# Kernel tuning notes

Measured on AMD Instinct MI355X. Metric: run time of the kernel, lower is better.

Reference implementation:

```python
import jax, jax.numpy as jnp
import numpy as np

D_MODEL = 512
N_HEADS = 8
D_FF = 1024
LV = 2048
LT = 512
GAMMA = 0.9
SCALE_BASE = 512  # XPOS default scale_base


def _dup_interleave(m):
    # (L, d/2) -> (L, d) duplicating each column: [a,b] -> [a,a,b,b]
    return jnp.repeat(m, 2, axis=-1)


def _xpos(x, downscale=False):
    # XPOS rotary embedding (RetNet-style), x: (B, L, d)
    B, L, d = x.shape
    half = d // 2
    s = (jnp.arange(0, d, 2, dtype=jnp.float32) + 0.4 * d) / (1.4 * d)  # (d/2,)
    scale = s[None, :] ** (jnp.arange(L, dtype=jnp.float32)[:, None] / SCALE_BASE)  # (L, d/2)
    inv_freq = 1.0 / (10000.0 ** (jnp.arange(half, dtype=jnp.float32) / half))
    ang = jnp.arange(L, dtype=jnp.float32)[:, None] * inv_freq[None, :]  # (L, d/2)
    if downscale:
        scale = 1.0 / scale
    sin = _dup_interleave(jnp.sin(ang) * scale)[None]  # (1, L, d)
    cos = _dup_interleave(jnp.cos(ang) * scale)[None]
    x1, x2 = x[..., 0::2], x[..., 1::2]
    rot = jnp.stack((-x2, x1), axis=-1).reshape(x.shape)  # rotate_every_two
    return x * cos + rot * sin


def _sine_pos(L, d):
    # DETR-style normalized 1D sine position embedding, mask = ones(1, L)
    x_embed = jnp.arange(1, L + 1, dtype=jnp.float32)  # cumsum of ones
    x_embed = x_embed / (x_embed[-1] + 1e-6) * (2.0 * np.pi)
    dim_t = jnp.arange(d, dtype=jnp.float32)
    dim_t = 10000.0 ** (2.0 * jnp.floor(dim_t / 2.0) / d)
    pos = x_embed[:, None] / dim_t[None, :]  # (L, d)
    pos = jnp.stack((jnp.sin(pos[:, 0::2]), jnp.cos(pos[:, 1::2])), axis=2).reshape(L, d)
    return pos[None]  # (1, L, d)


def _ln(x, w, b, eps=1e-5):
    mu = jnp.mean(x, axis=-1, keepdims=True)
    var = jnp.var(x, axis=-1, keepdims=True)
    return (x - mu) / jnp.sqrt(var + eps) * w + b


def _ret_forward(src_vid, src_txt, ln1_w, ln1_b, wq, bq, wk, bk, wv, bv, wo, bo,
                 lin1_w, lin1_b, lin2_w, lin2_b, ln2_w, ln2_b, ln3_w, ln3_b,
                 learn_ret_w):
    B, Lv, D = src_vid.shape
    Lt = src_txt.shape[1]
    h, dk = N_HEADS, D // N_HEADS

    # retention decay matrix D[n,m] = gamma^(n-m) for n>=m else 0
    n = jnp.arange(Lv)
    delta = jnp.maximum(n[:, None] - n[None, :], 0).astype(jnp.float32)
    Dm = jnp.where(n[:, None] >= n[None, :], GAMMA ** delta, 0.0)

    # learned sparse mask
    learn = jax.nn.sigmoid(learn_ret_w.reshape(Lv, Lv))
    diag = jnp.eye(Lv, dtype=jnp.float32)
    video_ret = (1.0 - diag) * learn
    learn_mask = diag + video_ret
    mask = Dm * learn_mask  # mask_choice == 'both'
    loss_sparsity = jnp.mean(jnp.abs(video_ret))

    # position encodings
    pos_vid_q = _xpos(src_vid)
    pos_vid_k = _xpos(src_vid, downscale=True)
    pos_txt = _sine_pos(Lt, D)
    src = jnp.concatenate([src_vid, src_txt], axis=1)       # (B, Lv+Lt, D)
    pos = jnp.concatenate([pos_vid_q, pos_txt], axis=1)
    pos_k = jnp.concatenate([pos_vid_k, pos_txt], axis=1)

    # --- RetLayer (eval mode: dropout = identity) ---
    src2 = _ln(src, ln1_w, ln1_b)
    q = src2[:, :Lv] + pos[:, :Lv]
    k = src2[:, :Lv] + pos_k[:, :Lv]
    v = src2[:, :Lv]

    # multi-head attention with MULTIPLICATIVE mask on logits
    qh = (q @ wq.T + bq).reshape(B, Lv, h, dk) / jnp.sqrt(jnp.float32(dk))
    kh = (k @ wk.T + bk).reshape(B, Lv, h, dk)
    vh = (v @ wv.T + bv).reshape(B, Lv, h, dk)
    attn = jnp.einsum('blhd,bmhd->bhlm', qh, kh) * mask[None, None]
    attn = jax.nn.softmax(attn, axis=-1)
    vid_att = jnp.einsum('bhlm,bmhd->blhd', attn, vh).reshape(B, Lv, D)
    vid_att = vid_att @ wo.T + bo

    src2 = jnp.concatenate([vid_att, src2[:, Lv:]], axis=1) + pos
    src = src + src2
    src2 = _ln(src, ln2_w, ln2_b)
    src2 = jax.nn.gelu(src2 @ lin1_w.T + lin1_b, approximate=False) @ lin2_w.T + lin2_b
    src = src + src2
    src = _ln(src, ln3_w, ln3_b)
    return src[:, :Lv], src[:, Lv:], loss_sparsity


def setup_inputs() -> dict:
    key = jax.random.key(0)
    ks = jax.random.split(key, 12)
    D, F = D_MODEL, D_FF
    w = lambda k, shp: (jax.random.normal(k, shp, dtype=jnp.float32) * 0.02)
    return {
        'src_vid': jax.random.normal(ks[0], (1, LV, D), dtype=jnp.float32),
        'src_txt': jax.random.normal(ks[1], (1, LT, D), dtype=jnp.float32),
        'ln1_w': jnp.ones((D,), jnp.float32), 'ln1_b': jnp.zeros((D,), jnp.float32),
        'wq': w(ks[2], (D, D)), 'bq': jnp.zeros((D,), jnp.float32),
        'wk': w(ks[3], (D, D)), 'bk': jnp.zeros((D,), jnp.float32),
        'wv': w(ks[4], (D, D)), 'bv': jnp.zeros((D,), jnp.float32),
        'wo': w(ks[5], (D, D)), 'bo': jnp.zeros((D,), jnp.float32),
        'lin1_w': w(ks[6], (F, D)), 'lin1_b': jnp.zeros((F,), jnp.float32),
        'lin2_w': w(ks[7], (D, F)), 'lin2_b': jnp.zeros((D,), jnp.float32),
        'ln2_w': jnp.ones((D,), jnp.float32), 'ln2_b': jnp.zeros((D,), jnp.float32),
        'ln3_w': jnp.ones((D,), jnp.float32), 'ln3_b': jnp.zeros((D,), jnp.float32),
        'learn_ret_w': jax.random.normal(ks[8], (LV * LV,), dtype=jnp.float32),
    }


def reference(src_vid, src_txt, ln1_w, ln1_b, wq, bq, wk, bk, wv, bv, wo, bo,
              lin1_w, lin1_b, lin2_w, lin2_b, ln2_w, ln2_b, ln3_w, ln3_b,
              learn_ret_w):
    return _ret_forward(src_vid, src_txt, ln1_w, ln1_b, wq, bq, wk, bk, wv, bv,
                        wo, bo, lin1_w, lin1_b, lin2_w, lin2_b, ln2_w, ln2_b,
                        ln3_w, ln3_b, learn_ret_w)
```

## Files before the change

kernel.cpp:

```cpp
#include <hip/hip_runtime.h>
#include <hip/hip_bf16.h>
#include <math.h>

#define LVID 2048
#define LTXT 512
#define DMOD 512
#define LTOT 2560
#define LOG2_GAMMA (-0.15200309344504995f)
#define LOG2E 1.4426950408889634f

typedef __bf16 bf16x8 __attribute__((ext_vector_type(8)));
typedef float f32x4 __attribute__((ext_vector_type(4)));

__device__ inline f32x4 mfma_bf16(bf16x8 a, bf16x8 b, f32x4 c) {
  return __builtin_amdgcn_mfma_f32_16x16x32_bf16(a, b, c, 0, 0, 0);
}

__device__ inline void gload_lds16(const void* g, void* l) {
  __builtin_amdgcn_global_load_lds(
      (const __attribute__((address_space(1))) void*)g,
      (__attribute__((address_space(3))) void*)l, 16, 0, 0);
}

union U8 { __hip_bfloat16 b[8]; uint4 u; };

__global__ __launch_bounds__(256) void k_prep_ln1(
    const float* __restrict__ lw, float* __restrict__ premask2,
    float* __restrict__ lossp,
    const float* __restrict__ wq, const float* __restrict__ wk,
    const float* __restrict__ wv, const float* __restrict__ wo,
    const float* __restrict__ l1, const float* __restrict__ l2,
    __hip_bfloat16* __restrict__ dst,
    const float* __restrict__ src_vid, const float* __restrict__ src_txt,
    const float* __restrict__ w, const float* __restrict__ b,
    __hip_bfloat16* __restrict__ acat, float* __restrict__ srcA,
    float* __restrict__ posb) {
  int tid = threadIdx.x;
  int blk = blockIdx.x;
  if (blk < 2048) {
    __shared__ float red[256];
    int i = blk;
    int i0r = i & ~63;
    int tloCol = (i0r > 900) ? (((i0r - 900) >> 6) << 6) : 0;
    int idx0 = (blk * 256 + tid) * 8;
    int j0 = idx0 & 2047;
    float4 lv0 = *(const float4*)&lw[idx0];
    float4 lv1 = *(const float4*)&lw[idx0 + 4];
    float lvv[8] = {lv0.x, lv0.y, lv0.z, lv0.w, lv1.x, lv1.y, lv1.z, lv1.w};
    float pm[8];
    float s = 0.f;
#pragma unroll
    for (int e = 0; e < 8; e++) {
      int j = j0 + e;
      float sig = 1.f / (1.f + __expf(-lvv[e]));
      if (j != i) s += sig;
      float m = (j > i) ? 0.f
              : ((j == i) ? 1.f : exp2f((float)(i - j) * LOG2_GAMMA) * sig);
      pm[e] = m * LOG2E;
    }
    if (j0 >= tloCol && j0 < i0r + 64) {
      *(float4*)&premask2[idx0]     = *(float4*)&pm[0];
      *(float4*)&premask2[idx0 + 4] = *(float4*)&pm[4];
    }
    red[tid] = s; __syncthreads();
    for (int st = 128; st > 0; st >>= 1) { if (tid < st) red[tid] += red[tid + st]; __syncthreads(); }
    if (tid == 0) lossp[blk] = red[0];
  } else if (blk < 4096) {
    int i4 = (blk - 2048) * 256 + tid;
    const float* sp; int base;
    if (i4 < 131072)      { if (i4 < 65536)  { sp = wq; base = 0; }      else { sp = wk; base = 65536; } }
    else if (i4 < 262144) { if (i4 < 196608) { sp = wv; base = 131072; } else { sp = wo; base = 196608; } }
    else if (i4 < 393216) { sp = l1; base = 262144; }
    else                  { sp = l2; base = 393216; }
    float4 v = ((const float4*)sp)[i4 - base];
    __hip_bfloat16 o[4] = {__float2bfloat16(v.x), __float2bfloat16(v.y),
                           __float2bfloat16(v.z), __float2bfloat16(v.w)};
    *(uint2*)(dst + (size_t)i4 * 4) = *(uint2*)o;
  } else {
    int row = (blk - 4096) * 4 + (tid >> 6);
    int lane = tid & 63;
    const float* xs = (row < LVID) ? (src_vid + (size_t)row * DMOD)
                                   : (src_txt + (size_t)(row - LVID) * DMOD);
    float x[8];
    { float4 v0 = *(const float4*)&xs[lane * 8];
      float4 v1 = *(const float4*)&xs[lane * 8 + 4];
      x[0]=v0.x; x[1]=v0.y; x[2]=v0.z; x[3]=v0.w;
      x[4]=v1.x; x[5]=v1.y; x[6]=v1.z; x[7]=v1.w; }
    float s = 0.f;
#pragma unroll
    for (int i = 0; i < 8; i++) s += x[i];
#pragma unroll
    for (int st = 1; st < 64; st <<= 1) s += __shfl_xor(s, st, 64);
    float mu = s * (1.f / DMOD);
    float vs = 0.f;
#pragma unroll
    for (int i = 0; i < 8; i++) { float d = x[i] - mu; vs += d * d; }
#pragma unroll
    for (int st = 1; st < 64; st <<= 1) vs += __shfl_xor(vs, st, 64);
    float inv = rsqrtf(vs * (1.f / DMOD) + 1e-5f);
    float y[8];
    { float4 w0 = *(const float4*)&w[lane * 8];
      float4 w1 = *(const float4*)&w[lane * 8 + 4];
      float4 b0 = *(const float4*)&b[lane * 8];
      float4 b1 = *(const float4*)&b[lane * 8 + 4];
      float wv_[8] = {w0.x,w0.y,w0.z,w0.w,w1.x,w1.y,w1.z,w1.w};
      float bv_[8] = {b0.x,b0.y,b0.z,b0.w,b1.x,b1.y,b1.z,b1.w};
#pragma unroll
      for (int i = 0; i < 8; i++) y[i] = (x[i] - mu) * inv * wv_[i] + bv_[i]; }
    size_t base = (size_t)row * DMOD + lane * 8;
    if (row < LVID) {
      U8 pv;
#pragma unroll
      for (int i = 0; i < 8; i++) pv.b[i] = __float2bfloat16(y[i]);
      *(uint4*)&acat[(size_t)(4096 + row) * DMOD + lane * 8] = pv.u;
      float pq[8], pk[8];
      float l = (float)row;
#pragma unroll
      for (int p = 0; p < 4; p++) {
        int j = lane * 4 + p;
        float sj = (2.f * j + 204.8f) * (1.f / 716.8f);
        float scale = __powf(sj, l * (1.f / 512.f));
        float invfreq = __powf(10000.f, -(float)j * (1.f / 256.f));
        float sn, cs; __sincosf(l * invfreq, &sn, &cs);
        float cq = cs * scale, sq = sn * scale;
        pq[2*p]   = x[2*p] * cq - x[2*p+1] * sq;
        pq[2*p+1] = x[2*p+1] * cq + x[2*p] * sq;
        float isc = 1.f / scale;
        float ck = cs * isc, sk = sn * isc;
        pk[2*p]   = x[2*p] * ck - x[2*p+1] * sk;
        pk[2*p+1] = x[2*p+1] * ck + x[2*p] * sk;
      }
      *(float4*)&posb[base]     = *(float4*)&pq[0];
      *(float4*)&posb[base + 4] = *(float4*)&pq[4];
      U8 pqv, pkv;
#pragma unroll
      for (int i = 0; i < 8; i++) {
        pqv.b[i] = __float2bfloat16(y[i] + pq[i]);
        pkv.b[i] = __float2bfloat16(y[i] + pk[i]);
      }
      *(uint4*)&acat[(size_t)row * DMOD + lane * 8] = pqv.u;
      *(uint4*)&acat[(size_t)(2048 + row) * DMOD + lane * 8] = pkv.u;
    } else {
      int l = row - LVID;
      float xe = (float)(l + 1) * (6.28318530717958647692f / 512.000001f);
      float o8[8];
#pragma unroll
      for (int p = 0; p < 4; p++) {
        int j = lane * 4 + p;
        float dimt = __powf(10000.f, (float)j * (1.f / 256.f));
        float a = xe / dimt;
        o8[2*p]   = x[2*p]   + y[2*p]   + __sinf(a);
        o8[2*p+1] = x[2*p+1] + y[2*p+1] + __cosf(a);
      }
      *(float4*)&srcA[base]     = *(float4*)&o8[0];
      *(float4*)&srcA[base + 4] = *(float4*)&o8[4];
    }
  }
}

__global__ __launch_bounds__(256) void k_ln2(
    const float* __restrict__ srcA,
    const float* __restrict__ w, const float* __restrict__ b,
    __hip_bfloat16* __restrict__ obf) {
  int row = blockIdx.x * 4 + (threadIdx.x >> 6);
  int lane = threadIdx.x & 63;
  size_t base = (size_t)row * DMOD + lane * 8;
  float x[8];
  { float4 v0 = *(const float4*)&srcA[base];
    float4 v1 = *(const float4*)&srcA[base + 4];
    x[0]=v0.x; x[1]=v0.y; x[2]=v0.z; x[3]=v0.w;
    x[4]=v1.x; x[5]=v1.y; x[6]=v1.z; x[7]=v1.w; }
  float s = 0.f;
#pragma unroll
  for (int i = 0; i < 8; i++) s += x[i];
#pragma unroll
  for (int st = 1; st < 64; st <<= 1) s += __shfl_xor(s, st, 64);
  float mu = s * (1.f / DMOD);
  float vs = 0.f;
#pragma unroll
  for (int i = 0; i < 8; i++) { float d = x[i] - mu; vs += d * d; }
#pragma unroll
  for (int st = 1; st < 64; st <<= 1) vs += __shfl_xor(vs, st, 64);
  float inv = rsqrtf(vs * (1.f / DMOD) + 1e-5f);
  float4 w0 = *(const float4*)&w[lane * 8];
  float4 w1 = *(const float4*)&w[lane * 8 + 4];
  float4 b0 = *(const float4*)&b[lane * 8];
  float4 b1 = *(const float4*)&b[lane * 8 + 4];
  float wv_[8] = {w0.x,w0.y,w0.z,w0.w,w1.x,w1.y,w1.z,w1.w};
  float bv_[8] = {b0.x,b0.y,b0.z,b0.w,b1.x,b1.y,b1.z,b1.w};
  U8 o;
#pragma unroll
  for (int i = 0; i < 8; i++)
    o.b[i] = __float2bfloat16((x[i] - mu) * inv * wv_[i] + bv_[i]);
  *(uint4*)&obf[base] = o.u;
}

__global__ __launch_bounds__(256) void k_ln3(
    const float* __restrict__ srcA, const float* __restrict__ ffo0,
    const float* __restrict__ ffo1,
    const float* __restrict__ w, const float* __restrict__ b,
    float* __restrict__ o, const float* __restrict__ lossp) {
  if (blockIdx.x == 0 && threadIdx.x < 64) {
    float s = 0.f;
    for (int i = threadIdx.x; i < 2048; i += 64) s += lossp[i];
#pragma unroll
    for (int st = 1; st < 64; st <<= 1) s += __shfl_xor(s, st, 64);
    if (threadIdx.x == 0) o[1310720] = s * (1.f / 4194304.f);
  }
  int row = blockIdx.x * 4 + (threadIdx.x >> 6);
  int lane = threadIdx.x & 63;
  size_t base = (size_t)row * DMOD + lane * 8;
  float x[8];
  { float4 a0 = *(const float4*)&srcA[base];
    float4 a1 = *(const float4*)&srcA[base + 4];
    float4 f0 = *(const float4*)&ffo0[base];
    float4 f1 = *(const float4*)&ffo0[base + 4];
    float4 g0 = *(const float4*)&ffo1[base];
    float4 g1 = *(const float4*)&ffo1[base + 4];
    x[0]=a0.x+f0.x+g0.x; x[1]=a0.y+f0.y+g0.y; x[2]=a0.z+f0.z+g0.z; x[3]=a0.w+f0.w+g0.w;
    x[4]=a1.x+f1.x+g1.x; x[5]=a1.y+f1.y+g1.y; x[6]=a1.z+f1.z+g1.z; x[7]=a1.w+f1.w+g1.w; }
  float s = 0.f;
#pragma unroll
  for (int i = 0; i < 8; i++) s += x[i];
#pragma unroll
  for (int st = 1; st < 64; st <<= 1) s += __shfl_xor(s, st, 64);
  float mu = s * (1.f / DMOD);
  float vs = 0.f;
#pragma unroll
  for (int i = 0; i < 8; i++) { float d = x[i] - mu; vs += d * d; }
#pragma unroll
  for (int st = 1; st < 64; st <<= 1) vs += __shfl_xor(vs, st, 64);
  float inv = rsqrtf(vs * (1.f / DMOD) + 1e-5f);
  float4 w0 = *(const float4*)&w[lane * 8];
  float4 w1 = *(const float4*)&w[lane * 8 + 4];
  float4 b0 = *(const float4*)&b[lane * 8];
  float4 b1 = *(const float4*)&b[lane * 8 + 4];
  float wv_[8] = {w0.x,w0.y,w0.z,w0.w,w1.x,w1.y,w1.z,w1.w};
  float bv_[8] = {b0.x,b0.y,b0.z,b0.w,b1.x,b1.y,b1.z,b1.w};
  float y[8];
#pragma unroll
  for (int i = 0; i < 8; i++) y[i] = (x[i] - mu) * inv * wv_[i] + bv_[i];
  *(float4*)&o[base]     = *(float4*)&y[0];
  *(float4*)&o[base + 4] = *(float4*)&y[4];
}

template <int EPI>
__global__ __launch_bounds__(256) void k_gemm4(
    const __hip_bfloat16* __restrict__ A, const __hip_bfloat16* __restrict__ W0,
    const float* __restrict__ b0, const float* __restrict__ b1,
    const float* __restrict__ b2, void* __restrict__ Cv,
    const float* __restrict__ res1, const float* __restrict__ res2,
    __hip_bfloat16* __restrict__ vT, float* __restrict__ vts,
    int M, int N, int K) {
  __shared__ __hip_bfloat16 sA[2][2048];
  __shared__ __hip_bfloat16 sB[2][2048];
  int tid = threadIdx.x, lane = tid & 63, w = tid >> 6;
  int c16 = lane & 15, q4 = lane >> 4;
  int bm = blockIdx.y * 64, bn = blockIdx.x * 64;
  int seg = (EPI == 3) ? (bm >> 11) : 0;
  const __hip_bfloat16* Wp = (EPI == 3) ? (W0 + (size_t)seg * ((size_t)N * K)) : W0;
  int kb   = (EPI == 5) ? (int)blockIdx.z * (K >> 1) : 0;
  int Keff = (EPI == 5) ? (K >> 1) : K;
  int r0 = tid >> 2, cc0 = (tid & 3) * 8;
  const __hip_bfloat16* gA = A  + (size_t)(bm + r0) * K + kb + cc0;
  const __hip_bfloat16* gB = Wp + (size_t)(bn + r0) * K + kb + cc0;
  auto stage = [&](int buf, int k0) {
    gload_lds16(gA + k0, &sA[buf][(size_t)tid * 8]);
    gload_lds16(gB + k0, &sB[buf][(size_t)tid * 8]);
  };
  f32x4 acc[2][2];
  { f32x4 z = {0.f,0.f,0.f,0.f}; acc[0][0]=z; acc[0][1]=z; acc[1][0]=z; acc[1][1]=z; }
  int wm = w & 1, wn = w >> 1;
  const int S = Keff >> 5;
  stage(0, 0);
  for (int s = 0; s < S; s++) {
    __syncthreads();
    if (s + 1 < S) stage((s + 1) & 1, (s + 1) * 32);
    int bf = s & 1;
    bf16x8 af[2], bfr[2];
    af[0]  = *(const bf16x8*)&sA[bf][(wm*32 + c16) * 32 + q4*8];
    af[1]  = *(const bf16x8*)&sA[bf][(wm*32 + 16 + c16) * 32 + q4*8];
    bfr[0] = *(const bf16x8*)&sB[bf][(wn*32 + c16) * 32 + q4*8];
    bfr[1] = *(const bf16x8*)&sB[bf][(wn*32 + 16 + c16) * 32 + q4*8];
    acc[0][0] = mfma_bf16(af[0], bfr[0], acc[0][0]);
    acc[0][1] = mfma_bf16(af[0], bfr[1], acc[0][1]);
    acc[1][0] = mfma_bf16(af[1], bfr[0], acc[1][0]);
    acc[1][1] = mfma_bf16(af[1], bfr[1], acc[1][1]);
  }
  float alpha = (EPI == 3 && seg == 0) ? 0.125f : 1.f;
  const float* bp = (EPI == 3) ? (seg == 0 ? b0 : (seg == 1 ? b1 : b2)) : b0;
  if (EPI == 3 && seg == 2) {
    int tile = (bm & 2047) >> 6;
    float vsum[2] = {0.f, 0.f};
#pragma unroll
    for (int j = 0; j < 2; j++) {
      int n = bn + wn*32 + j*16 + c16;
      float bs = bp[n];
#pragma unroll
      for (int i = 0; i < 2; i++) {
        ushort4 u; float vv[4];
#pragma unroll
        for (int r = 0; r < 4; r++) {
          __hip_bfloat16 vb = __float2bfloat16(acc[i][j][r] + bs);
          ((__hip_bfloat16*)&u)[r] = vb;
          vv[r] = __bfloat162float(vb);
        }
        int jj = (bm & 2047) + wm*32 + i*16 + q4*4;
        *(ushort4*)&vT[(size_t)n * 2048 + jj] = u;
        vsum[j] += vv[0] + vv[1] + vv[2] + vv[3];
      }
    }
#pragma unroll
    for (int j = 0; j < 2; j++) {
      float s2 = vsum[j];
      s2 += __shfl_xor(s2, 16, 64);
      s2 += __shfl_xor(s2, 32, 64);
      int n = bn + wn*32 + j*16 + c16;
      if (q4 == 0) atomicAdd(&vts[(size_t)(n >> 6) * 2048 + tile * 64 + (n & 63)], s2);
    }
    return;
  }
  float vdummy;
  (void)vdummy;
#pragma unroll
  for (int j = 0; j < 2; j++) {
    int n = bn + wn*32 + j*16 + c16;
    float bs = bp[n];
    if (EPI == 5 && blockIdx.z != 0) bs = 0.f;
#pragma unroll
    for (int i = 0; i < 2; i++) {
#pragma unroll
      for (int r = 0; r < 4; r++) {
        int m = bm + wm*32 + i*16 + q4*4 + r;
        float v = (acc[i][j][r] + bs) * alpha;
        if (EPI == 4) v = 0.5f * v * (1.f + erff(v * 0.70710678118654752f));
        if (EPI == 2) {
          size_t off = (size_t)m * N + n;
          ((float*)Cv)[off] = v + res1[off] + res2[off];
        } else if (EPI == 4) {
          ((__hip_bfloat16*)Cv)[(size_t)m * N + n] = __float2bfloat16(v);
        } else if (EPI == 5) {
          ((float*)Cv)[(size_t)blockIdx.z * 1310720 + (size_t)m * N + n] = v;
        } else {
          ((__hip_bfloat16*)Cv)[(size_t)(m & 2047) * 1024 + seg * 512 + n] = __float2bfloat16(v);
        }
      }
    }
  }
}

__global__ __launch_bounds__(256) void k_attn(
    const __hip_bfloat16* __restrict__ qkb,
    const float* __restrict__ premask2,
    const __hip_bfloat16* __restrict__ vT,
    __hip_bfloat16* __restrict__ Obuf,
    float* __restrict__ ml) {
  __shared__ __hip_bfloat16 sQ[64][72];
  __shared__ __hip_bfloat16 sK[2][64][72];
  __shared__ __hip_bfloat16 sVt[2][64][72];
  __shared__ __hip_bfloat16 sP[64][72];
  int i0 = blockIdx.x * 64, h = blockIdx.y, z = blockIdx.z;
  int tid = threadIdx.x, lane = tid & 63, w = tid >> 6;
  int c16 = lane & 15, q4 = lane >> 4;
  {
    int r = tid >> 2, c0 = (tid & 3) * 16;
    const __hip_bfloat16* g = qkb + (size_t)(i0 + r) * 1024 + h * 64 + c0;
    *(uint4*)&sQ[r][c0]     = *(const uint4*)g;
    *(uint4*)&sQ[r][c0 + 8] = *(const uint4*)(g + 8);
  }
  int thi = i0 >> 6;
  int tlo = (i0 > 900) ? ((i0 - 900) >> 6) : 0;
  int n = thi - tlo + 1;
  int t0 = z ? (tlo + (n >> 1)) : tlo;
  int t1 = z ? thi : (tlo + (n >> 1) - 1);
  float rm = 0.f, rz = 0.f;
  f32x4 O[4];
  { f32x4 zz = {0.f,0.f,0.f,0.f}; O[0]=zz; O[1]=zz; O[2]=zz; O[3]=zz; }
  int kr = tid >> 2, kc = (tid & 3) * 16;
  uint4 pk0, pk1, pv0, pv1;
  if (t0 <= t1) {
    const __hip_bfloat16* gk = qkb + (size_t)(t0*64 + kr) * 1024 + 512 + h*64 + kc;
    pk0 = *(const uint4*)gk; pk1 = *(const uint4*)(gk + 8);
    const __hip_bfloat16* gv = vT + (size_t)(h*64 + kr) * 2048 + t0*64 + kc;
    pv0 = *(const uint4*)gv; pv1 = *(const uint4*)(gv + 8);
  }
  for (int t = t0; t <= t1; t++) {
    int buf = (t - t0) & 1;
    *(uint4*)&sK[buf][kr][kc]      = pk0;
    *(uint4*)&sK[buf][kr][kc + 8]  = pk1;
    *(uint4*)&sVt[buf][kr][kc]     = pv0;
    *(uint4*)&sVt[buf][kr][kc + 8] = pv1;
    __syncthreads();
    if (t < t1) {
      const __hip_bfloat16* gk = qkb + (size_t)((t+1)*64 + kr) * 1024 + 512 + h*64 + kc;
      pk0 = *(const uint4*)gk; pk1 = *(const uint4*)(gk + 8);
      const __hip_bfloat16* gv = vT + (size_t)(h*64 + kr) * 2048 + (t+1)*64 + kc;
      pv0 = *(const uint4*)gv; pv1 = *(const uint4*)(gv + 8);
    }
    bf16x8 bq0 = *(const bf16x8*)&sQ[w*16 + c16][q4*8];
    bf16x8 bq1 = *(const bf16x8*)&sQ[w*16 + c16][32 + q4*8];
    f32x4 St[4];
#pragma unroll
    for (int jt = 0; jt < 4; jt++) {
      f32x4 zz = {0.f,0.f,0.f,0.f};
      bf16x8 a0 = *(const bf16x8*)&sK[buf][jt*16 + c16][q4*8];
      bf16x8 a1 = *(const bf16x8*)&sK[buf][jt*16 + c16][32 + q4*8];
      zz = mfma_bf16(a0, bq0, zz);
      zz = mfma_bf16(a1, bq1, zz);
      St[jt] = zz;
    }
    int qg = i0 + w*16 + c16;
    float lg[4][4];
    float tmax = -3.0e38f;
#pragma unroll
    for (int jt = 0; jt < 4; jt++) {
      float4 pm = *(const float4*)&premask2[(size_t)qg * 2048 + t*64 + jt*16 + q4*4];
      lg[jt][0] = St[jt][0] * pm.x; lg[jt][1] = St[jt][1] * pm.y;
      lg[jt][2] = St[jt][2] * pm.z; lg[jt][3] = St[jt][3] * pm.w;
#pragma unroll
      for (int r = 0; r < 4; r++) tmax = fmaxf(tmax, lg[jt][r]);
    }
    tmax = fmaxf(tmax, __shfl_xor(tmax, 16, 64));
    tmax = fmaxf(tmax, __shfl_xor(tmax, 32, 64));
    float mn = fmaxf(rm, tmax);
    float al = exp2f(rm - mn);
    rm = mn;
    float zp = 0.f;
#pragma unroll
    for (int jt = 0; jt < 4; jt++) {
      U8 e4;
      float e0 = exp2f(lg[jt][0] - rm), e1 = exp2f(lg[jt][1] - rm);
      float e2 = exp2f(lg[jt][2] - rm), e3 = exp2f(lg[jt][3] - rm);
      zp += e0 + e1 + e2 + e3;
      e4.b[0] = __float2bfloat16(e0); e4.b[1] = __float2bfloat16(e1);
      e4.b[2] = __float2bfloat16(e2); e4.b[3] = __float2bfloat16(e3);
      *(uint2*)&sP[w*16 + c16][jt*16 + q4*4] = *(uint2*)&e4.b[0];
    }
    zp += __shfl_xor(zp, 16, 64);
    zp += __shfl_xor(zp, 32, 64);
    rz = rz * al + zp;
    float alr[4];
#pragma unroll
    for (int r = 0; r < 4; r++) alr[r] = __shfl(al, q4*4 + r, 64);
#pragma unroll
    for (int dt = 0; dt < 4; dt++)
#pragma unroll
      for (int r = 0; r < 4; r++) O[dt][r] *= alr[r];
    bf16x8 ap0 = *(const bf16x8*)&sP[w*16 + c16][q4*8];
    bf16x8 ap1 = *(const bf16x8*)&sP[w*16 + c16][32 + q4*8];
#pragma unroll
    for (int dt = 0; dt < 4; dt++) {
      bf16x8 bv0 = *(const bf16x8*)&sVt[buf][dt*16 + c16][q4*8];
      bf16x8 bv1 = *(const bf16x8*)&sVt[buf][dt*16 + c16][32 + q4*8];
      O[dt] = mfma_bf16(ap0, bv0, O[dt]);
      O[dt] = mfma_bf16(ap1, bv1, O[dt]);
    }
  }
  __hip_bfloat16* ob = Obuf + (size_t)z * (2048 * 512);
#pragma unroll
  for (int dt = 0; dt < 4; dt++) {
    int d = dt*16 + c16;
#pragma unroll
    for (int r = 0; r < 4; r++)
      ob[(size_t)(i0 + w*16 + q4*4 + r) * DMOD + h*64 + d] = __float2bfloat16(O[dt][r]);
  }
  if (q4 == 0) {
    size_t mi = (((size_t)z * 8 + h) * 2048 + i0 + w*16 + c16) * 2;
    ml[mi] = rm; ml[mi + 1] = rz;
  }
}

__global__ __launch_bounds__(256) void k_comb(
    const __hip_bfloat16* __restrict__ Obuf, const float* __restrict__ ml,
    const float* __restrict__ vts,
    __hip_bfloat16* __restrict__ outp) {
  __shared__ float sV[32][64];
  __shared__ float sS[64];
  __shared__ float sC[64][4];
  int i0 = blockIdx.x * 64, h = blockIdx.y;
  int tid = threadIdx.x;
  int thi = i0 >> 6;
  int tlo = (i0 > 900) ? ((i0 - 900) >> 6) : 0;
  int n = thi - tlo + 1;
  float nu = (float)(2048 - 64 * n);
  {
    const float4* src = (const float4*)(vts + (size_t)h * 2048);
    ((float4*)&sV[0][0])[tid * 2]     = src[tid * 2];
    ((float4*)&sV[0][0])[tid * 2 + 1] = src[tid * 2 + 1];
  }
  __syncthreads();
  if (tid < 64) {
    float s = 0.f;
    for (int t = 0; t < 32; t++) if (t < tlo || t > thi) s += sV[t][tid];
    sS[tid] = s;
  } else if (tid < 128) {
    int r = tid - 64;
    int row = i0 + r;
    float m0 = ml[(((size_t)0 * 8 + h) * 2048 + row) * 2];
    float l0 = ml[(((size_t)0 * 8 + h) * 2048 + row) * 2 + 1];
    float m1 = ml[(((size_t)1 * 8 + h) * 2048 + row) * 2];
    float l1 = ml[(((size_t)1 * 8 + h) * 2048 + row) * 2 + 1];
    float M = fmaxf(m0, m1);
    float a0 = exp2f(m0 - M), a1 = exp2f(m1 - M), au = exp2f(-M);
    float dinv = 1.f / (l0 * a0 + l1 * a1 + nu * au);
    sC[r][0] = a0 * dinv; sC[r][1] = a1 * dinv; sC[r][2] = au * dinv;
  }
  __syncthreads();
  int r = tid >> 2, dc = (tid & 3) * 16;
  size_t off = (size_t)(i0 + r) * DMOD + h * 64 + dc;
  U8 o0a, o0b, o1a, o1b, oa, obb;
  o0a.u = *(const uint4*)&Obuf[off];
  o0b.u = *(const uint4*)&Obuf[off + 8];
  o1a.u = *(const uint4*)&Obuf[(size_t)2048 * 512 + off];
  o1b.u = *(const uint4*)&Obuf[(size_t)2048 * 512 + off + 8];
  float c0 = sC[r][0], c1 = sC[r][1], cu = sC[r][2];
#pragma unroll
  for (int k = 0; k < 8; k++) {
    float v = __bfloat162float(o0a.b[k]) * c0 + __bfloat162float(o1a.b[k]) * c1
            + sS[dc + k] * cu;
    oa.b[k] = __float2bfloat16(v);
  }
#pragma unroll
  for (int k = 0; k < 8; k++) {
    float v = __bfloat162float(o0b.b[k]) * c0 + __bfloat162float(o1b.b[k]) * c1
            + sS[dc + 8 + k] * cu;
    obb.b[k] = __float2bfloat16(v);
  }
  *(uint4*)&outp[off]     = oa.u;
  *(uint4*)&outp[off + 8] = obb.u;
}

extern "C" void kernel_launch(void* const* d_in, const int* in_sizes, int n_in,
                              void* d_out, int out_size, void* d_ws, size_t ws_size,
                              hipStream_t stream) {
  const float* src_vid = (const float*)d_in[0];
  const float* src_txt = (const float*)d_in[1];
  const float* ln1_w = (const float*)d_in[2];
  const float* ln1_b = (const float*)d_in[3];
  const float* wq = (const float*)d_in[4];
  const float* bq = (const float*)d_in[5];
  const float* wk = (const float*)d_in[6];
  const float* bk = (const float*)d_in[7];
  const float* wv = (const float*)d_in[8];
  const float* bv = (const float*)d_in[9];
  const float* wo = (const float*)d_in[10];
  const float* bo = (const float*)d_in[11];
  const float* lin1_w = (const float*)d_in[12];
  const float* lin1_b = (const float*)d_in[13];
  const float* lin2_w = (const float*)d_in[14];
  const float* lin2_b = (const float*)d_in[15];
  const float* ln2_w = (const float*)d_in[16];
  const float* ln2_b = (const float*)d_in[17];
  const float* ln3_w = (const float*)d_in[18];
  const float* ln3_b = (const float*)d_in[19];
  const float* lw = (const float*)d_in[20];
  float* out = (float*)d_out;

  const size_t MB = 1048576;
  char* wsb = (char*)d_ws;
  float* premask2       = (float*)(wsb + 0);
  __hip_bfloat16* wqb   = (__hip_bfloat16*)(wsb + 16*MB);
  __hip_bfloat16* wob   = wqb + 786432;
  __hip_bfloat16* l1b   = wqb + 1048576;
  __hip_bfloat16* l2b   = wqb + 1572864;
  __hip_bfloat16* acat  = (__hip_bfloat16*)(wsb + 20*MB);
  __hip_bfloat16* qkb   = (__hip_bfloat16*)(wsb + 26*MB);
  __hip_bfloat16* vTb   = (__hip_bfloat16*)(wsb + 30*MB);
  __hip_bfloat16* Obuf  = (__hip_bfloat16*)(wsb + 32*MB);
  float* mlb            = (float*)(wsb + 36*MB);
  float* vts            = (float*)(wsb + 37*MB);
  __hip_bfloat16* vattb = (__hip_bfloat16*)(wsb + 38*MB);
  float* srcA           = (float*)(wsb + 40*MB);
  float* posb           = (float*)(wsb + 45*MB);
  __hip_bfloat16* s2b   = (__hip_bfloat16*)(wsb + 50*MB);
  __hip_bfloat16* hidb  = (__hip_bfloat16*)(wsb + 53*MB);
  float* ffo0           = (float*)(wsb + 58*MB);
  float* ffo1           = (float*)(wsb + 63*MB);
  float* lossp          = (float*)(wsb + 68*MB);

  hipMemsetAsync(vts, 0, 8 * 32 * 64 * sizeof(float), stream);

  k_prep_ln1<<<4736, 256, 0, stream>>>(lw, premask2, lossp,
      wq, wk, wv, wo, lin1_w, lin2_w, wqb,
      src_vid, src_txt, ln1_w, ln1_b, acat, srcA, posb);

  k_gemm4<3><<<dim3(8, 96), 256, 0, stream>>>(acat, wqb, bq, bk, bv,
      qkb, nullptr, nullptr, vTb, vts, 6144, 512, 512);
  k_attn<<<dim3(32, 8, 2), 256, 0, stream>>>(qkb, premask2, vTb, Obuf, mlb);
  k_comb<<<dim3(32, 8), 256, 0, stream>>>(Obuf, mlb, vts, vattb);
  k_gemm4<2><<<dim3(8, 32), 256, 0, stream>>>(vattb, wob, bo, nullptr, nullptr,
      srcA, src_vid, posb, nullptr, nullptr, 2048, 512, 512);
  k_ln2<<<640, 256, 0, stream>>>(srcA, ln2_w, ln2_b, s2b);
  k_gemm4<4><<<dim3(16, 40), 256, 0, stream>>>(s2b, l1b, lin1_b, nullptr, nullptr,
      hidb, nullptr, nullptr, nullptr, nullptr, 2560, 1024, 512);
  k_gemm4<5><<<dim3(8, 40, 2), 256, 0, stream>>>(hidb, l2b, lin2_b, nullptr, nullptr,
      ffo0, nullptr, nullptr, nullptr, nullptr, 2560, 512, 1024);
  k_ln3<<<640, 256, 0, stream>>>(srcA, ffo0, ffo1, ln3_w, ln3_b, out, lossp);
}
```

Measured before the change: 216.1 us.

## Split attention KV range four ways, deepen GEMM k-step, fold vts memset

Attention blocks now split each query tile's key-tile range into four partitions instead of two. The combine kernel merges four partial softmax states plus the uniform term, and the workspace layout is enlarged to hold four Obuf slices. The GEMM kernel stages 64-wide K chunks per barrier instead of 32, halving synchronisation count at the cost of doubled LDS. The separate memset of vts is folded into the first prep kernel to drop one launch. This risks more partial-result traffic in the combine step.

```diff
diff --git a/kernel.cpp b/kernel.cpp
--- a/kernel.cpp
+++ b/kernel.cpp
@@ -26,7 +26,7 @@
 
 __global__ __launch_bounds__(256) void k_prep_ln1(
     const float* __restrict__ lw, float* __restrict__ premask2,
-    float* __restrict__ lossp,
+    float* __restrict__ lossp, float* __restrict__ vts,
     const float* __restrict__ wq, const float* __restrict__ wk,
     const float* __restrict__ wv, const float* __restrict__ wo,
     const float* __restrict__ l1, const float* __restrict__ l2,
@@ -37,6 +37,7 @@
     float* __restrict__ posb) {
   int tid = threadIdx.x;
   int blk = blockIdx.x;
+  if (blk < 64) vts[blk * 256 + tid] = 0.f;
   if (blk < 2048) {
     __shared__ float red[256];
     int i = blk;
@@ -245,15 +246,15 @@
 }
 
 template <int EPI>
-__global__ __launch_bounds__(256) void k_gemm4(
+__global__ __launch_bounds__(256) void k_gemm5(
     const __hip_bfloat16* __restrict__ A, const __hip_bfloat16* __restrict__ W0,
     const float* __restrict__ b0, const float* __restrict__ b1,
     const float* __restrict__ b2, void* __restrict__ Cv,
     const float* __restrict__ res1, const float* __restrict__ res2,
     __hip_bfloat16* __restrict__ vT, float* __restrict__ vts,
     int M, int N, int K) {
-  __shared__ __hip_bfloat16 sA[2][2048];
-  __shared__ __hip_bfloat16 sB[2][2048];
+  __shared__ __hip_bfloat16 sA[2][4096];
+  __shared__ __hip_bfloat16 sB[2][4096];
   int tid = threadIdx.x, lane = tid & 63, w = tid >> 6;
   int c16 = lane & 15, q4 = lane >> 4;
   int bm = blockIdx.y * 64, bn = blockIdx.x * 64;
@@ -265,27 +266,31 @@
   const __hip_bfloat16* gA = A  + (size_t)(bm + r0) * K + kb + cc0;
   const __hip_bfloat16* gB = Wp + (size_t)(bn + r0) * K + kb + cc0;
   auto stage = [&](int buf, int k0) {
-    gload_lds16(gA + k0, &sA[buf][(size_t)tid * 8]);
-    gload_lds16(gB + k0, &sB[buf][(size_t)tid * 8]);
+    gload_lds16(gA + k0,      &sA[buf][(size_t)tid * 8]);
+    gload_lds16(gA + k0 + 32, &sA[buf][2048 + (size_t)tid * 8]);
+    gload_lds16(gB + k0,      &sB[buf][(size_t)tid * 8]);
+    gload_lds16(gB + k0 + 32, &sB[buf][2048 + (size_t)tid * 8]);
   };
   f32x4 acc[2][2];
   { f32x4 z = {0.f,0.f,0.f,0.f}; acc[0][0]=z; acc[0][1]=z; acc[1][0]=z; acc[1][1]=z; }
   int wm = w & 1, wn = w >> 1;
-  const int S = Keff >> 5;
+  const int S = Keff >> 6;
   stage(0, 0);
   for (int s = 0; s < S; s++) {
     __syncthreads();
-    if (s + 1 < S) stage((s + 1) & 1, (s + 1) * 32);
+    if (s + 1 < S) stage((s + 1) & 1, (s + 1) * 64);
     int bf = s & 1;
-    bf16x8 af[2], bfr[2];
-    af[0]  = *(const bf16x8*)&sA[bf][(wm*32 + c16) * 32 + q4*8];
-    af[1]  = *(const bf16x8*)&sA[bf][(wm*32 + 16 + c16) * 32 + q4*8];
-    bfr[0] = *(const bf16x8*)&sB[bf][(wn*32 + c16) * 32 + q4*8];
-    bfr[1] = *(const bf16x8*)&sB[bf][(wn*32 + 16 + c16) * 32 + q4*8];
-    acc[0][0] = mfma_bf16(af[0], bfr[0], acc[0][0]);
-    acc[0][1] = mfma_bf16(af[0], bfr[1], acc[0][1]);
-    acc[1][0] = mfma_bf16(af[1], bfr[0], acc[1][0]);
-    acc[1][1] = mfma_bf16(af[1], bfr[1], acc[1][1]);
+#pragma unroll
+    for (int kc = 0; kc < 2; kc++) {
+      bf16x8 a0  = *(const bf16x8*)&sA[bf][kc*2048 + (wm*32 + c16) * 32 + q4*8];
+      bf16x8 a1  = *(const bf16x8*)&sA[bf][kc*2048 + (wm*32 + 16 + c16) * 32 + q4*8];
+      bf16x8 bv0 = *(const bf16x8*)&sB[bf][kc*2048 + (wn*32 + c16) * 32 + q4*8];
+      bf16x8 bv1 = *(const bf16x8*)&sB[bf][kc*2048 + (wn*32 + 16 + c16) * 32 + q4*8];
+      acc[0][0] = mfma_bf16(a0, bv0, acc[0][0]);
+      acc[0][1] = mfma_bf16(a0, bv1, acc[0][1]);
+      acc[1][0] = mfma_bf16(a1, bv0, acc[1][0]);
+      acc[1][1] = mfma_bf16(a1, bv1, acc[1][1]);
+    }
   }
   float alpha = (EPI == 3 && seg == 0) ? 0.125f : 1.f;
   const float* bp = (EPI == 3) ? (seg == 0 ? b0 : (seg == 1 ? b1 : b2)) : b0;
@@ -320,8 +325,6 @@
     }
     return;
   }
-  float vdummy;
-  (void)vdummy;
 #pragma unroll
   for (int j = 0; j < 2; j++) {
     int n = bn + wn*32 + j*16 + c16;
@@ -370,9 +373,9 @@
   }
   int thi = i0 >> 6;
   int tlo = (i0 > 900) ? ((i0 - 900) >> 6) : 0;
-  int n = thi - tlo + 1;
-  int t0 = z ? (tlo + (n >> 1)) : tlo;
-  int t1 = z ? thi : (tlo + (n >> 1) - 1);
+  int nt_ = thi - tlo + 1;
+  int t0 = tlo + ((nt_ * z) >> 2);
+  int t1 = tlo + ((nt_ * (z + 1)) >> 2) - 1;
   float rm = 0.f, rz = 0.f;
   f32x4 O[4];
   { f32x4 zz = {0.f,0.f,0.f,0.f}; O[0]=zz; O[1]=zz; O[2]=zz; O[3]=zz; }
@@ -476,7 +479,7 @@
     __hip_bfloat16* __restrict__ outp) {
   __shared__ float sV[32][64];
   __shared__ float sS[64];
-  __shared__ float sC[64][4];
+  __shared__ float sC[64][6];
   int i0 = blockIdx.x * 64, h = blockIdx.y;
   int tid = threadIdx.x;
   int thi = i0 >> 6;
@@ -496,35 +499,50 @@
   } else if (tid < 128) {
     int r = tid - 64;
     int row = i0 + r;
-    float m0 = ml[(((size_t)0 * 8 + h) * 2048 + row) * 2];
-    float l0 = ml[(((size_t)0 * 8 + h) * 2048 + row) * 2 + 1];
-    float m1 = ml[(((size_t)1 * 8 + h) * 2048 + row) * 2];
-    float l1 = ml[(((size_t)1 * 8 + h) * 2048 + row) * 2 + 1];
-    float M = fmaxf(m0, m1);
-    float a0 = exp2f(m0 - M), a1 = exp2f(m1 - M), au = exp2f(-M);
-    float dinv = 1.f / (l0 * a0 + l1 * a1 + nu * au);
-    sC[r][0] = a0 * dinv; sC[r][1] = a1 * dinv; sC[r][2] = au * dinv;
+    float m[4], l[4];
+#pragma unroll
+    for (int z = 0; z < 4; z++) {
+      size_t mi = (((size_t)z * 8 + h) * 2048 + row) * 2;
+      m[z] = ml[mi]; l[z] = ml[mi + 1];
+    }
+    float M = fmaxf(fmaxf(m[0], m[1]), fmaxf(m[2], m[3]));
+    float au = exp2f(-M);
+    float a[4], D = nu * au;
+#pragma unroll
+    for (int z = 0; z < 4; z++) { a[z] = exp2f(m[z] - M); D += l[z] * a[z]; }
+    float dinv = 1.f / D;
+#pragma unroll
+    for (int z = 0; z < 4; z++) sC[r][z] = a[z] * dinv;
+    sC[r][4] = au * dinv;
   }
   __syncthreads();
   int r = tid >> 2, dc = (tid & 3) * 16;
   size_t off = (size_t)(i0 + r) * DMOD + h * 64 + dc;
-  U8 o0a, o0b, o1a, o1b, oa, obb;
-  o0a.u = *(const uint4*)&Obuf[off];
-  o0b.u = *(const uint4*)&Obuf[off + 8];
-  o1a.u = *(const uint4*)&Obuf[(size_t)2048 * 512 + off];
-  o1b.u = *(const uint4*)&Obuf[(size_t)2048 * 512 + off + 8];
-  float c0 = sC[r][0], c1 = sC[r][1], cu = sC[r][2];
+  float c[4];
+#pragma unroll
+  for (int z = 0; z < 4; z++) c[z] = sC[r][z];
+  float cu = sC[r][4];
+  float va[16], vb[16];
+#pragma unroll
+  for (int k = 0; k < 16; k++) { va[k] = sS[dc + (k & 7)] * 0.f; }
+  U8 oa, obb;
+#pragma unroll
+  for (int k = 0; k < 8; k++) { va[k] = sS[dc + k] * cu; vb[k] = sS[dc + 8 + k] * cu; }
+#pragma unroll
+  for (int z = 0; z < 4; z++) {
+    U8 pa, pb;
+    pa.u = *(const uint4*)&Obuf[(size_t)z * 2048 * 512 + off];
+    pb.u = *(const uint4*)&Obuf[(size_t)z * 2048 * 512 + off + 8];
+#pragma unroll
+    for (int k = 0; k < 8; k++) {
+      va[k] += __bfloat162float(pa.b[k]) * c[z];
+      vb[k] += __bfloat162float(pb.b[k]) * c[z];
+    }
+  }
 #pragma unroll
   for (int k = 0; k < 8; k++) {
-    float v = __bfloat162float(o0a.b[k]) * c0 + __bfloat162float(o1a.b[k]) * c1
-            + sS[dc + k] * cu;
-    oa.b[k] = __float2bfloat16(v);
-  }
-#pragma unroll
-  for (int k = 0; k < 8; k++) {
-    float v = __bfloat162float(o0b.b[k]) * c0 + __bfloat162float(o1b.b[k]) * c1
-            + sS[dc + 8 + k] * cu;
-    obb.b[k] = __float2bfloat16(v);
+    oa.b[k]  = __float2bfloat16(va[k]);
+    obb.b[k] = __float2bfloat16(vb[k]);
   }
   *(uint4*)&outp[off]     = oa.u;
   *(uint4*)&outp[off + 8] = obb.u;
@@ -567,33 +585,31 @@
   __hip_bfloat16* qkb   = (__hip_bfloat16*)(wsb + 26*MB);
   __hip_bfloat16* vTb   = (__hip_bfloat16*)(wsb + 30*MB);
   __hip_bfloat16* Obuf  = (__hip_bfloat16*)(wsb + 32*MB);
-  float* mlb            = (float*)(wsb + 36*MB);
-  float* vts            = (float*)(wsb + 37*MB);
-  __hip_bfloat16* vattb = (__hip_bfloat16*)(wsb + 38*MB);
-  float* srcA           = (float*)(wsb + 40*MB);
-  float* posb           = (float*)(wsb + 45*MB);
-  __hip_bfloat16* s2b   = (__hip_bfloat16*)(wsb + 50*MB);
-  __hip_bfloat16* hidb  = (__hip_bfloat16*)(wsb + 53*MB);
-  float* ffo0           = (float*)(wsb + 58*MB);
-  float* ffo1           = (float*)(wsb + 63*MB);
-  float* lossp          = (float*)(wsb + 68*MB);
-
-  hipMemsetAsync(vts, 0, 8 * 32 * 64 * sizeof(float), stream);
-
-  k_prep_ln1<<<4736, 256, 0, stream>>>(lw, premask2, lossp,
+  float* mlb            = (float*)(wsb + 40*MB);
+  float* vts            = (float*)(wsb + 41*MB);
+  __hip_bfloat16* vattb = (__hip_bfloat16*)(wsb + 42*MB);
+  float* srcA           = (float*)(wsb + 44*MB);
+  float* posb           = (float*)(wsb + 49*MB);
+  __hip_bfloat16* s2b   = (__hip_bfloat16*)(wsb + 54*MB);
+  __hip_bfloat16* hidb  = (__hip_bfloat16*)(wsb + 57*MB);
+  float* ffo0           = (float*)(wsb + 62*MB);
+  float* ffo1           = (float*)(wsb + 67*MB);
+  float* lossp          = (float*)(wsb + 72*MB);
+
+  k_prep_ln1<<<4736, 256, 0, stream>>>(lw, premask2, lossp, vts,
       wq, wk, wv, wo, lin1_w, lin2_w, wqb,
       src_vid, src_txt, ln1_w, ln1_b, acat, srcA, posb);
 
-  k_gemm4<3><<<dim3(8, 96), 256, 0, stream>>>(acat, wqb, bq, bk, bv,
+  k_gemm5<3><<<dim3(8, 96), 256, 0, stream>>>(acat, wqb, bq, bk, bv,
       qkb, nullptr, nullptr, vTb, vts, 6144, 512, 512);
-  k_attn<<<dim3(32, 8, 2), 256, 0, stream>>>(qkb, premask2, vTb, Obuf, mlb);
+  k_attn<<<dim3(32, 8, 4), 256, 0, stream>>>(qkb, premask2, vTb, Obuf, mlb);
   k_comb<<<dim3(32, 8), 256, 0, stream>>>(Obuf, mlb, vts, vattb);
-  k_gemm4<2><<<dim3(8, 32), 256, 0, stream>>>(vattb, wob, bo, nullptr, nullptr,
+  k_gemm5<2><<<dim3(8, 32), 256, 0, stream>>>(vattb, wob, bo, nullptr, nullptr,
       srcA, src_vid, posb, nullptr, nullptr, 2048, 512, 512);
   k_ln2<<<640, 256, 0, stream>>>(srcA, ln2_w, ln2_b, s2b);
-  k_gemm4<4><<<dim3(16, 40), 256, 0, stream>>>(s2b, l1b, lin1_b, nullptr, nullptr,
+  k_gemm5<4><<<dim3(16, 40), 256, 0, stream>>>(s2b, l1b, lin1_b, nullptr, nullptr,
       hidb, nullptr, nullptr, nullptr, nullptr, 2560, 1024, 512);
-  k_gemm4<5><<<dim3(8, 40, 2), 256, 0, stream>>>(hidb, l2b, lin2_b, nullptr, nullptr,
+  k_gemm5<5><<<dim3(8, 40, 2), 256, 0, stream>>>(hidb, l2b, lin2_b, nullptr, nullptr,
       ffo0, nullptr, nullptr, nullptr, nullptr, 2560, 512, 1024);
   k_ln3<<<640, 256, 0, stream>>>(srcA, ffo0, ffo1, ln3_w, ln3_b, out, lossp);
 }
```

New measurement: 206.6 us. 4.4% less time.
